# Performance work log

Hardware: AMD Instinct MI355X
Metric: run time of the kernel (lower is better)

## Reference

```python
import jax, jax.numpy as jnp
import numpy as np

B, N, D, H = 2, 2048, 1024, 16
DH = D // H


def setup_inputs() -> dict:
    key = jax.random.key(0)
    ks = jax.random.split(key, 5)
    s = 0.02
    return {
        "x": jax.random.normal(ks[0], (B, N, D), dtype=jnp.float32),
        "Wq": jax.random.normal(ks[1], (D, D), dtype=jnp.float32) * s,
        "Wk": jax.random.normal(ks[2], (D, D), dtype=jnp.float32) * s,
        "Wv": jax.random.normal(ks[3], (D, D), dtype=jnp.float32) * s,
        "Wo": jax.random.normal(ks[4], (D, D), dtype=jnp.float32) * s,
        "bo": jnp.zeros((D,), dtype=jnp.float32),
    }


def reference(x, Wq, Wk, Wv, Wo, bo):
    b, n, d = x.shape
    # linear projections (torch Linear: y = x @ W.T), split into heads -> [b,h,n,dh]
    def proj(W):
        return jnp.einsum('bnd,ed->bne', x, W).reshape(b, n, H, DH).transpose(0, 2, 1, 3)
    q, k, v = proj(Wq), proj(Wk), proj(Wv)
    scores = jnp.einsum('bhqd,bhkd->bhqk', q, k)  # [b,h,n,n]
    causal = jnp.triu(jnp.ones((n, n), dtype=bool), k=1)
    scores = jnp.where(causal, -jnp.inf, scores)
    # NOTE: module scales by 1/sqrt(num_key_tokens), not 1/sqrt(d_head)
    w = jax.nn.softmax(scores / jnp.sqrt(jnp.float32(n)), axis=-1)
    ctx = jnp.einsum('bhqk,bhkd->bhqd', w, v)
    ctx = ctx.transpose(0, 2, 1, 3).reshape(b, n, d)
    return jnp.einsum('bnd,ed->bne', ctx, Wo) + bo
```

## Files before the change

kernel.cpp:

```cpp
#include <hip/hip_runtime.h>
#include <hip/hip_bf16.h>

typedef __attribute__((ext_vector_type(8))) short bf16x8;
typedef __attribute__((ext_vector_type(4))) float f32x4;
typedef __attribute__((ext_vector_type(16))) float f32x16;
typedef unsigned short u16;
typedef unsigned int u32;

__device__ __forceinline__ u16 f2bf(float f) {
  union { float f; unsigned int u; } v; v.f = f;
  return (u16)((v.u + 0x7fffu + ((v.u >> 16) & 1u)) >> 16);
}
__device__ __forceinline__ u32 pack_bf2(float f0, float f1) {
  union { float f; unsigned int u; } a, b; a.f = f0; b.f = f1;
  return __builtin_amdgcn_perm(b.u + 0x8000u, a.u + 0x8000u, 0x07060302u);
}

#define GLOAD_LDS16(g, l) __builtin_amdgcn_global_load_lds( \
    (const __attribute__((address_space(1))) void*)(g),     \
    (__attribute__((address_space(3))) void*)(l), 16, 0, 0)

__global__ __launch_bounds__(256) void conv_all(const float* __restrict__ x,
                                                const float* __restrict__ wq, const float* __restrict__ wk,
                                                const float* __restrict__ wv, const float* __restrict__ wo,
                                                u16* __restrict__ xb, u16* __restrict__ qo, u16* __restrict__ ko,
                                                u16* __restrict__ vo, u16* __restrict__ oo) {
  int y = blockIdx.y;
  const float* src; u16* dst;
  if (y < 4) { src = x + (size_t)y * 1048576; dst = xb + (size_t)y * 1048576; }
  else if (y == 4) { src = wq; dst = qo; }
  else if (y == 5) { src = wk; dst = ko; }
  else if (y == 6) { src = wv; dst = vo; }
  else { src = wo; dst = oo; }
  int i = (blockIdx.x * 256 + threadIdx.x) * 4;
  float4 v = *(const float4*)(src + i);
  ushort4 o;
  o.x = f2bf(v.x); o.y = f2bf(v.y); o.z = f2bf(v.z); o.w = f2bf(v.w);
  *(ushort4*)(dst + i) = o;
}

template <bool SW>
__device__ __forceinline__ void gemm_main(const u16* __restrict__ A, const u16* __restrict__ W,
                                          u16* As, u16* Bs, int m0, int n0, int K,
                                          f32x4 acc[4][4]) {
  int tid = threadIdx.x, wave = tid >> 6, lane = tid & 63;
  int lane15 = lane & 15, quad = lane >> 4;
  int wm = (wave >> 1) * 64, wn = (wave & 1) * 64;
  for (int k0 = 0; k0 < K; k0 += 64) {
    __syncthreads();
#pragma unroll
    for (int i = 0; i < 4; i++) {
      int rbase = wave * 32 + i * 8;
      int rloc = rbase + (lane >> 3);
      int ca = ((lane & 7) ^ (rloc & 7)) * 8;
      GLOAD_LDS16(A + (size_t)(m0 + rloc) * K + k0 + ca, As + rbase * 64);
      GLOAD_LDS16(W + (size_t)(n0 + rloc) * K + k0 + ca, Bs + rbase * 64);
    }
    __syncthreads();
#pragma unroll
    for (int kc = 0; kc < 2; kc++) {
      bf16x8 a[4], b[4];
#pragma unroll
      for (int mi = 0; mi < 4; mi++) {
        int m = wm + mi * 16 + lane15;
        a[mi] = *(const bf16x8*)(As + m * 64 + (((kc * 4 + quad) ^ (m & 7)) * 8));
      }
#pragma unroll
      for (int ni = 0; ni < 4; ni++) {
        int n = wn + ni * 16 + lane15;
        b[ni] = *(const bf16x8*)(Bs + n * 64 + (((kc * 4 + quad) ^ (n & 7)) * 8));
      }
#pragma unroll
      for (int mi = 0; mi < 4; mi++)
#pragma unroll
        for (int ni = 0; ni < 4; ni++)
          acc[mi][ni] = SW ? __builtin_amdgcn_mfma_f32_16x16x32_bf16(b[ni], a[mi], acc[mi][ni], 0, 0, 0)
                           : __builtin_amdgcn_mfma_f32_16x16x32_bf16(a[mi], b[ni], acc[mi][ni], 0, 0, 0);
    }
  }
}

__global__ __launch_bounds__(256, 3) void gemm_qkv(const u16* __restrict__ xb,
                                                   const u16* __restrict__ wq, const u16* __restrict__ wk,
                                                   const u16* __restrict__ wv,
                                                   u16* __restrict__ Qb, u16* __restrict__ Kb,
                                                   u16* __restrict__ Vtg) {
  __shared__ __align__(16) u16 As[128 * 64];
  __shared__ __align__(16) u16 Bs[128 * 64];
  const int K = 1024;
  int z = blockIdx.z;
  const u16* W = (z == 0) ? wq : (z == 1) ? wk : wv;
  int m0 = blockIdx.x * 128, n0 = blockIdx.y * 128;
  f32x4 acc[4][4];
#pragma unroll
  for (int i = 0; i < 4; i++)
#pragma unroll
    for (int j = 0; j < 4; j++) acc[i][j] = (f32x4){0.f, 0.f, 0.f, 0.f};

  int tid = threadIdx.x, wave = tid >> 6, lane = tid & 63;
  int lane15 = lane & 15, quad = lane >> 4;
  int wm = (wave >> 1) * 64, wn = (wave & 1) * 64;
  const float kQs = 0.022097086912079608f * 1.4426950408889634f;

  if (z < 2) {
    gemm_main<true>(xb, W, As, Bs, m0, n0, K, acc);
    u16* Out = z ? Kb : Qb;
    float sc = z ? 1.0f : kQs;
#pragma unroll
    for (int mi = 0; mi < 4; mi++)
#pragma unroll
      for (int ni = 0; ni < 4; ni++) {
        int token = m0 + wm + mi * 16 + lane15;
        int fb = n0 + wn + ni * 16 + quad * 4;
        ushort4 o;
        o.x = f2bf(acc[mi][ni][0] * sc); o.y = f2bf(acc[mi][ni][1] * sc);
        o.z = f2bf(acc[mi][ni][2] * sc); o.w = f2bf(acc[mi][ni][3] * sc);
        *(ushort4*)&Out[(size_t)token * 1024 + fb] = o;
      }
  } else {
    gemm_main<false>(xb, W, As, Bs, m0, n0, K, acc);
#pragma unroll
    for (int mi = 0; mi < 4; mi++)
#pragma unroll
      for (int ni = 0; ni < 4; ni++) {
        int row = m0 + wm + mi * 16 + quad * 4;
        int col = n0 + wn + ni * 16 + lane15;
        int bb = row >> 11, nn = row & 2047;
        ushort4 o;
        o.x = f2bf(acc[mi][ni][0]); o.y = f2bf(acc[mi][ni][1]);
        o.z = f2bf(acc[mi][ni][2]); o.w = f2bf(acc[mi][ni][3]);
        *(ushort4*)&Vtg[(size_t)(bb * 1024 + col) * 2048 + nn] = o;
      }
  }
}

__global__ __launch_bounds__(256, 2) void gemm_out(const u16* __restrict__ A, const u16* __restrict__ W,
                                                   float* __restrict__ Of, const float* __restrict__ bias) {
  __shared__ __align__(16) u16 As[128 * 64];
  __shared__ __align__(16) u16 Bs[64 * 64];
  const int K = 1024;
  int m0 = blockIdx.x * 128, n0 = blockIdx.y * 64;
  int tid = threadIdx.x, wave = tid >> 6, lane = tid & 63;
  int lane15 = lane & 15, quad = lane >> 4;
  int wm = (wave >> 1) * 64, wn = (wave & 1) * 32;
  f32x4 acc[4][2];
#pragma unroll
  for (int i = 0; i < 4; i++)
#pragma unroll
    for (int j = 0; j < 2; j++) acc[i][j] = (f32x4){0.f, 0.f, 0.f, 0.f};
  for (int k0 = 0; k0 < K; k0 += 64) {
    __syncthreads();
#pragma unroll
    for (int i = 0; i < 4; i++) {
      int rbase = wave * 32 + i * 8;
      int rloc = rbase + (lane >> 3);
      int ca = ((lane & 7) ^ (rloc & 7)) * 8;
      GLOAD_LDS16(A + (size_t)(m0 + rloc) * K + k0 + ca, As + rbase * 64);
    }
#pragma unroll
    for (int i = 0; i < 2; i++) {
      int rbase = wave * 16 + i * 8;
      int rloc = rbase + (lane >> 3);
      int ca = ((lane & 7) ^ (rloc & 7)) * 8;
      GLOAD_LDS16(W + (size_t)(n0 + rloc) * K + k0 + ca, Bs + rbase * 64);
    }
    __syncthreads();
#pragma unroll
    for (int kc = 0; kc < 2; kc++) {
      bf16x8 a[4], b[2];
#pragma unroll
      for (int mi = 0; mi < 4; mi++) {
        int m = wm + mi * 16 + lane15;
        a[mi] = *(const bf16x8*)(As + m * 64 + (((kc * 4 + quad) ^ (m & 7)) * 8));
      }
#pragma unroll
      for (int ni = 0; ni < 2; ni++) {
        int n = wn + ni * 16 + lane15;
        b[ni] = *(const bf16x8*)(Bs + n * 64 + (((kc * 4 + quad) ^ (n & 7)) * 8));
      }
#pragma unroll
      for (int mi = 0; mi < 4; mi++)
#pragma unroll
        for (int ni = 0; ni < 2; ni++)
          acc[mi][ni] = __builtin_amdgcn_mfma_f32_16x16x32_bf16(b[ni], a[mi], acc[mi][ni], 0, 0, 0);
    }
  }
#pragma unroll
  for (int mi = 0; mi < 4; mi++)
#pragma unroll
    for (int ni = 0; ni < 2; ni++) {
      int token = m0 + wm + mi * 16 + lane15;
      int fb = n0 + wn + ni * 16 + quad * 4;
      float4 bb = *(const float4*)&bias[fb];
      float4 o;
      o.x = acc[mi][ni][0] + bb.x; o.y = acc[mi][ni][1] + bb.y;
      o.z = acc[mi][ni][2] + bb.z; o.w = acc[mi][ni][3] + bb.w;
      *(float4*)&Of[(size_t)token * 1024 + fb] = o;
    }
}

__global__ __launch_bounds__(256, 2) void attn8(const u16* __restrict__ Q, const u16* __restrict__ Kg,
                                                const u16* __restrict__ Vtg, u16* __restrict__ ctx) {
  __shared__ __align__(16) u16 SH[16384];
  int tid = threadIdx.x, wave = tid >> 6, lane = tid & 63;
  int l31 = lane & 31, hf = lane >> 5;
  int qt = wave;

  int bh = blockIdx.x, by = blockIdx.y;
  int sidx = (by < 8) ? (15 - by) : (by - 8);
  int b = bh >> 4, h = bh & 15;
  int qbase = sidx * 128;
  int qw = qbase + qt * 32;
  int gq = qw + l31;

  bf16x8 qb[4];
#pragma unroll
  for (int s = 0; s < 4; s++)
    qb[s] = *(const bf16x8*)&Q[(size_t)(b * 2048 + gq) * 1024 + h * 64 + s * 16 + hf * 8];

  f32x16 oacc[2];
#pragma unroll
  for (int dt = 0; dt < 2; dt++)
#pragma unroll
    for (int r = 0; r < 16; r++) oacc[dt][r] = 0.f;
  float lsum = 0.f;

  auto stage = [&](int t, int d) {
    int tb = t * 64;
    u16* Kd = SH + d * 4096;
    u16* Vd = SH + 8192 + d * 4096;
#pragma unroll
    for (int i = 0; i < 2; i++) {
      int rbase = wave * 16 + i * 8;
      int rk = rbase + (lane >> 3);
      int ca = ((lane & 7) ^ (rk & 7)) * 8;
      GLOAD_LDS16(&Kg[(size_t)(b * 2048 + tb + rk) * 1024 + h * 64 + ca], Kd + rbase * 64);
      GLOAD_LDS16(&Vtg[(size_t)(b * 1024 + h * 64 + rk) * 2048 + tb + ca], Vd + rbase * 64);
    }
  };

  int tmax = 2 * sidx + 1;
  stage(0, 0);
  for (int t = 0; t <= tmax; ++t) {
    __syncthreads();
    if (t < tmax) stage(t + 1, (t + 1) & 1);
    if (t * 64 > qw + 31) continue;
    int d = t & 1;
    const u16* Kd = SH + d * 4096;
    const u16* Vd = SH + 8192 + d * 4096;

    const u16* kp0 = Kd + l31 * 64;
    const u16* kp1 = Kd + (32 + l31) * 64;
    bf16x8 kf0[4], kf1[4];
#pragma unroll
    for (int s = 0; s < 4; s++) {
      int sw = ((2 * s + hf) ^ (l31 & 7)) * 8;
      kf0[s] = *(const bf16x8*)(kp0 + sw);
      kf1[s] = *(const bf16x8*)(kp1 + sw);
    }

    f32x16 sv0, sv1;
#pragma unroll
    for (int r = 0; r < 16; r++) { sv0[r] = 0.f; sv1[r] = 0.f; }
    __builtin_amdgcn_s_setprio(1);
#pragma unroll
    for (int s = 0; s < 4; s++) {
      sv0 = __builtin_amdgcn_mfma_f32_32x32x16_bf16(kf0[s], qb[s], sv0, 0, 0, 0);
      sv1 = __builtin_amdgcn_mfma_f32_32x32x16_bf16(kf1[s], qb[s], sv1, 0, 0, 0);
    }
    __builtin_amdgcn_s_setprio(0);

    if (t * 64 + 63 > qw) {
#pragma unroll
      for (int r = 0; r < 16; r++) {
        int kv = t * 64 + (r & 3) + 8 * (r >> 2) + 4 * hf;
        if (kv > gq) sv0[r] = -10000.0f;
        if (kv + 32 > gq) sv1[r] = -10000.0f;
      }
    }
#pragma unroll
    for (int r = 0; r < 16; r++) {
      float p = __builtin_amdgcn_exp2f(sv0[r]); sv0[r] = p; lsum += p;
    }
#pragma unroll
    for (int r = 0; r < 16; r++) {
      float p = __builtin_amdgcn_exp2f(sv1[r]); sv1[r] = p; lsum += p;
    }

    union U8 { u32 u[4]; bf16x8 v; };
    U8 pf[4];
    {
      u32 p0 = pack_bf2(sv0[0], sv0[1]),   p1 = pack_bf2(sv0[2], sv0[3]);
      u32 p2 = pack_bf2(sv0[4], sv0[5]),   p3 = pack_bf2(sv0[6], sv0[7]);
      u32 p4 = pack_bf2(sv0[8], sv0[9]),   p5 = pack_bf2(sv0[10], sv0[11]);
      u32 p6 = pack_bf2(sv0[12], sv0[13]), p7 = pack_bf2(sv0[14], sv0[15]);
      u32 x0 = __shfl_xor(hf ? p0 : p2, 32);
      u32 x1 = __shfl_xor(hf ? p1 : p3, 32);
      u32 x2 = __shfl_xor(hf ? p4 : p6, 32);
      u32 x3 = __shfl_xor(hf ? p5 : p7, 32);
      pf[0].u[0] = hf ? x0 : p0; pf[0].u[1] = hf ? x1 : p1;
      pf[0].u[2] = hf ? p2 : x0; pf[0].u[3] = hf ? p3 : x1;
      pf[1].u[0] = hf ? x2 : p4; pf[1].u[1] = hf ? x3 : p5;
      pf[1].u[2] = hf ? p6 : x2; pf[1].u[3] = hf ? p7 : x3;
    }
    {
      u32 p0 = pack_bf2(sv1[0], sv1[1]),   p1 = pack_bf2(sv1[2], sv1[3]);
      u32 p2 = pack_bf2(sv1[4], sv1[5]),   p3 = pack_bf2(sv1[6], sv1[7]);
      u32 p4 = pack_bf2(sv1[8], sv1[9]),   p5 = pack_bf2(sv1[10], sv1[11]);
      u32 p6 = pack_bf2(sv1[12], sv1[13]), p7 = pack_bf2(sv1[14], sv1[15]);
      u32 x0 = __shfl_xor(hf ? p0 : p2, 32);
      u32 x1 = __shfl_xor(hf ? p1 : p3, 32);
      u32 x2 = __shfl_xor(hf ? p4 : p6, 32);
      u32 x3 = __shfl_xor(hf ? p5 : p7, 32);
      pf[2].u[0] = hf ? x0 : p0; pf[2].u[1] = hf ? x1 : p1;
      pf[2].u[2] = hf ? p2 : x0; pf[2].u[3] = hf ? p3 : x1;
      pf[3].u[0] = hf ? x2 : p4; pf[3].u[1] = hf ? x3 : p5;
      pf[3].u[2] = hf ? p6 : x2; pf[3].u[3] = hf ? p7 : x3;
    }

    __builtin_amdgcn_s_setprio(1);
#pragma unroll
    for (int c = 0; c < 4; c++) {
#pragma unroll
      for (int dt = 0; dt < 2; dt++) {
        int vrow = dt * 32 + l31;
        bf16x8 va = *(const bf16x8*)(Vd + vrow * 64 + (((2 * c + hf) ^ (vrow & 7)) * 8));
        oacc[dt] = __builtin_amdgcn_mfma_f32_32x32x16_bf16(va, pf[c].v, oacc[dt], 0, 0, 0);
      }
    }
    __builtin_amdgcn_s_setprio(0);
  }

  lsum += __shfl_xor(lsum, 32);
  float inv = 1.0f / lsum;
  size_t off = (size_t)(b * 2048 + gq) * 1024 + h * 64;
#pragma unroll
  for (int dt = 0; dt < 2; dt++) {
#pragma unroll
    for (int gr = 0; gr < 4; gr++) {
      ushort4 o;
      o.x = f2bf(oacc[dt][4 * gr + 0] * inv);
      o.y = f2bf(oacc[dt][4 * gr + 1] * inv);
      o.z = f2bf(oacc[dt][4 * gr + 2] * inv);
      o.w = f2bf(oacc[dt][4 * gr + 3] * inv);
      *(ushort4*)&ctx[off + dt * 32 + 8 * gr + 4 * hf] = o;
    }
  }
}

extern "C" void kernel_launch(void* const* d_in, const int* in_sizes, int n_in,
                              void* d_out, int out_size, void* d_ws, size_t ws_size,
                              hipStream_t stream) {
  const float* x  = (const float*)d_in[0];
  const float* Wq = (const float*)d_in[1];
  const float* Wk = (const float*)d_in[2];
  const float* Wv = (const float*)d_in[3];
  const float* Wo = (const float*)d_in[4];
  const float* bo = (const float*)d_in[5];
  float* out = (float*)d_out;
  char* ws = (char*)d_ws;
  const size_t MB = 1024 * 1024;
  u16* xb   = (u16*)(ws);
  u16* wqb  = (u16*)(ws +  8 * MB);
  u16* wkb  = (u16*)(ws + 10 * MB);
  u16* wvb  = (u16*)(ws + 12 * MB);
  u16* wob  = (u16*)(ws + 14 * MB);
  u16* Qb   = (u16*)(ws + 16 * MB);
  u16* Kb   = (u16*)(ws + 24 * MB);
  u16* Vtg  = (u16*)(ws + 32 * MB);
  u16* ctxb = (u16*)(ws + 40 * MB);

  conv_all<<<dim3(1024, 8), 256, 0, stream>>>(x, Wq, Wk, Wv, Wo, xb, wqb, wkb, wvb, wob);
  gemm_qkv<<<dim3(32, 8, 3), 256, 0, stream>>>(xb, wqb, wkb, wvb, Qb, Kb, Vtg);
  attn8<<<dim3(32, 16), 256, 0, stream>>>(Qb, Kb, Vtg, ctxb);
  gemm_out<<<dim3(32, 16), 256, 0, stream>>>(ctxb, wob, out, bo);
}
```

Before: 169.5 us.

## Shrink attention blocks to 64 queries and skip fully-masked causal subtiles

The attention kernel now uses 2 waves per block, each covering 32 queries, so a block spans 64 queries and the grid doubles to 32 along y with a new heavy/light interleaved schedule. Each block loads only as many KV tiles as its causal range needs. Inside a tile, the second 32-key half is skipped (QK MFMAs, exp, packing and PV MFMAs) when it lies entirely above the diagonal. This removes wasted causal work and idle waves, at the cost of half as many waves sharing each staged KV tile and twice the global-to-LDS loads per wave.

Result: slower. 173.9 us (+2.6%).

```diff
diff --git a/kernel.cpp b/kernel.cpp
--- a/kernel.cpp
+++ b/kernel.cpp
@@ -199,18 +199,16 @@
     }
 }
 
-__global__ __launch_bounds__(256, 2) void attn8(const u16* __restrict__ Q, const u16* __restrict__ Kg,
+__global__ __launch_bounds__(128, 2) void attn9(const u16* __restrict__ Q, const u16* __restrict__ Kg,
                                                 const u16* __restrict__ Vtg, u16* __restrict__ ctx) {
   __shared__ __align__(16) u16 SH[16384];
   int tid = threadIdx.x, wave = tid >> 6, lane = tid & 63;
   int l31 = lane & 31, hf = lane >> 5;
-  int qt = wave;
 
   int bh = blockIdx.x, by = blockIdx.y;
-  int sidx = (by < 8) ? (15 - by) : (by - 8);
+  int sidx = (by < 8) ? (31 - by) : (by < 16) ? (by - 8) : (by < 24) ? (39 - by) : (by - 16);
   int b = bh >> 4, h = bh & 15;
-  int qbase = sidx * 128;
-  int qw = qbase + qt * 32;
+  int qw = sidx * 64 + wave * 32;
   int gq = qw + l31;
 
   bf16x8 qb[4];
@@ -230,8 +228,8 @@
     u16* Kd = SH + d * 4096;
     u16* Vd = SH + 8192 + d * 4096;
 #pragma unroll
-    for (int i = 0; i < 2; i++) {
-      int rbase = wave * 16 + i * 8;
+    for (int i = 0; i < 4; i++) {
+      int rbase = wave * 32 + i * 8;
       int rk = rbase + (lane >> 3);
       int ca = ((lane & 7) ^ (rk & 7)) * 8;
       GLOAD_LDS16(&Kg[(size_t)(b * 2048 + tb + rk) * 1024 + h * 64 + ca], Kd + rbase * 64);
@@ -239,15 +237,18 @@
     }
   };
 
-  int tmax = 2 * sidx + 1;
+  int tmax = sidx;
   stage(0, 0);
   for (int t = 0; t <= tmax; ++t) {
     __syncthreads();
     if (t < tmax) stage(t + 1, (t + 1) & 1);
-    if (t * 64 > qw + 31) continue;
     int d = t & 1;
     const u16* Kd = SH + d * 4096;
     const u16* Vd = SH + 8192 + d * 4096;
+
+    bool diag0 = (t * 64 + 31 > qw);
+    bool full1 = (t * 64 + 32 <= qw + 31);
+    bool diag1 = full1 && (t * 64 + 63 > qw);
 
     const u16* kp0 = Kd + l31 * 64;
     const u16* kp1 = Kd + (32 + l31) * 64;
@@ -264,27 +265,38 @@
     for (int r = 0; r < 16; r++) { sv0[r] = 0.f; sv1[r] = 0.f; }
     __builtin_amdgcn_s_setprio(1);
 #pragma unroll
-    for (int s = 0; s < 4; s++) {
+    for (int s = 0; s < 4; s++)
       sv0 = __builtin_amdgcn_mfma_f32_32x32x16_bf16(kf0[s], qb[s], sv0, 0, 0, 0);
-      sv1 = __builtin_amdgcn_mfma_f32_32x32x16_bf16(kf1[s], qb[s], sv1, 0, 0, 0);
+    if (full1) {
+#pragma unroll
+      for (int s = 0; s < 4; s++)
+        sv1 = __builtin_amdgcn_mfma_f32_32x32x16_bf16(kf1[s], qb[s], sv1, 0, 0, 0);
     }
     __builtin_amdgcn_s_setprio(0);
 
-    if (t * 64 + 63 > qw) {
+    if (diag0) {
 #pragma unroll
       for (int r = 0; r < 16; r++) {
         int kv = t * 64 + (r & 3) + 8 * (r >> 2) + 4 * hf;
         if (kv > gq) sv0[r] = -10000.0f;
-        if (kv + 32 > gq) sv1[r] = -10000.0f;
+      }
+    }
+    if (diag1) {
+#pragma unroll
+      for (int r = 0; r < 16; r++) {
+        int kv = t * 64 + 32 + (r & 3) + 8 * (r >> 2) + 4 * hf;
+        if (kv > gq) sv1[r] = -10000.0f;
       }
     }
 #pragma unroll
     for (int r = 0; r < 16; r++) {
       float p = __builtin_amdgcn_exp2f(sv0[r]); sv0[r] = p; lsum += p;
     }
-#pragma unroll
-    for (int r = 0; r < 16; r++) {
-      float p = __builtin_amdgcn_exp2f(sv1[r]); sv1[r] = p; lsum += p;
+    if (full1) {
+#pragma unroll
+      for (int r = 0; r < 16; r++) {
+        float p = __builtin_amdgcn_exp2f(sv1[r]); sv1[r] = p; lsum += p;
+      }
     }
 
     union U8 { u32 u[4]; bf16x8 v; };
@@ -303,7 +315,7 @@
       pf[1].u[0] = hf ? x2 : p4; pf[1].u[1] = hf ? x3 : p5;
       pf[1].u[2] = hf ? p6 : x2; pf[1].u[3] = hf ? p7 : x3;
     }
-    {
+    if (full1) {
       u32 p0 = pack_bf2(sv1[0], sv1[1]),   p1 = pack_bf2(sv1[2], sv1[3]);
       u32 p2 = pack_bf2(sv1[4], sv1[5]),   p3 = pack_bf2(sv1[6], sv1[7]);
       u32 p4 = pack_bf2(sv1[8], sv1[9]),   p5 = pack_bf2(sv1[10], sv1[11]);
@@ -320,12 +332,23 @@
 
     __builtin_amdgcn_s_setprio(1);
 #pragma unroll
-    for (int c = 0; c < 4; c++) {
+    for (int c = 0; c < 2; c++) {
 #pragma unroll
       for (int dt = 0; dt < 2; dt++) {
         int vrow = dt * 32 + l31;
         bf16x8 va = *(const bf16x8*)(Vd + vrow * 64 + (((2 * c + hf) ^ (vrow & 7)) * 8));
         oacc[dt] = __builtin_amdgcn_mfma_f32_32x32x16_bf16(va, pf[c].v, oacc[dt], 0, 0, 0);
+      }
+    }
+    if (full1) {
+#pragma unroll
+      for (int c = 2; c < 4; c++) {
+#pragma unroll
+        for (int dt = 0; dt < 2; dt++) {
+          int vrow = dt * 32 + l31;
+          bf16x8 va = *(const bf16x8*)(Vd + vrow * 64 + (((2 * c + hf) ^ (vrow & 7)) * 8));
+          oacc[dt] = __builtin_amdgcn_mfma_f32_32x32x16_bf16(va, pf[c].v, oacc[dt], 0, 0, 0);
+        }
       }
     }
     __builtin_amdgcn_s_setprio(0);
@@ -372,6 +395,6 @@
 
   conv_all<<<dim3(1024, 8), 256, 0, stream>>>(x, Wq, Wk, Wv, Wo, xb, wqb, wkb, wvb, wob);
   gemm_qkv<<<dim3(32, 8, 3), 256, 0, stream>>>(xb, wqb, wkb, wvb, Qb, Kb, Vtg);
-  attn8<<<dim3(32, 16), 256, 0, stream>>>(Qb, Kb, Vtg, ctxb);
+  attn9<<<dim3(32, 32), 128, 0, stream>>>(Qb, Kb, Vtg, ctxb);
   gemm_out<<<dim3(32, 16), 256, 0, stream>>>(ctxb, wob, out, bo);
 }
```
